# Kernel optimization log

Measured on AMD Instinct MI355X. Metric: run time of the kernel, lower is better.

The kernel has to match this reference:

```python
import jax, jax.numpy as jnp
import numpy as np

G, C_PER, C_IN, J, B, H, W, K = 8, 32, 256, 64, 16, 56, 56, 3


def setup_inputs() -> dict:
    key = jax.random.key(0)
    kx, kw, kb = jax.random.split(key, 3)
    x = jax.random.normal(kx, (B, C_IN, H, W), dtype=jnp.float32)
    # Per-cluster conv weights [G, j_rank, c, K, K] and biases [G, j_rank]
    weight = jax.random.normal(kw, (G, J, C_PER, K, K), dtype=jnp.float32) * 0.05
    bias = jax.random.normal(kb, (G, J), dtype=jnp.float32) * 0.01
    # Arrangements: 8 clusters of 32 non-contiguous channel indices (fixed permutation)
    arrangements = jnp.asarray(
        np.random.RandomState(0).permutation(C_IN).reshape(G, C_PER), dtype=jnp.int32
    )
    return {"x": x, "weight": weight, "bias": bias, "arrangements": arrangements}


def reference(x, weight, bias, arrangements):
    # Gather channel subsets: x[:, arr] -> [B, G, c, H, W] -> [G, B, c, H, W]
    xg = jnp.transpose(x[:, arrangements], (1, 0, 2, 3, 4))

    def conv1(xi, wi):
        # xi: [B, c, H, W], wi: [J, c, K, K]; stride 1, pad 1, dilation 1 (torch default cross-correlation)
        return jax.lax.conv_general_dilated(
            xi, wi,
            window_strides=(1, 1),
            padding=((1, 1), (1, 1)),
            dimension_numbers=("NCHW", "OIHW", "NCHW"),
        )

    out = jax.vmap(conv1)(xg, weight)              # [G, B, J, H, W]
    out = out + bias[:, None, :, None, None]
    g, b, j, h, w = out.shape
    # torch.cat(dim=1) over clusters -> [B, G*J, H, W]
    return jnp.transpose(out, (1, 0, 2, 3, 4)).reshape(b, g * j, h, w)
```

## Files before the change

### kernel.cpp

```cpp
#include <hip/hip_runtime.h>


#define NG 8
#define CPER 32
#define CIN 256
#define NJ 64
#define NB 16
#define NH 56
#define NW 56
#define PXST 40
#define BUFSH (4 * 58 * PXST)
#define NPACK (16 * 4 * 58)
#define NITER 15
#define WEI_SH (9 * 2048)

typedef __attribute__((ext_vector_type(8))) short short8v;
typedef __attribute__((ext_vector_type(4))) float float4v;

__device__ __forceinline__ unsigned bf16rne(float f) {
    unsigned u = __float_as_uint(f);
    return (u + 0x7FFFu + ((u >> 16) & 1u)) >> 16;
}

__global__ __launch_bounds__(256, 2)
void gconv_mfma(const float* __restrict__ x,
                const float* __restrict__ w,
                const float* __restrict__ bias,
                const int* __restrict__ arr,
                float* __restrict__ out) {
    __shared__ __align__(16) unsigned short smem[2 * BUFSH];

    const int tid   = threadIdx.x;
    const int chunk = blockIdx.x;
    const int b     = blockIdx.y;
    const int g     = blockIdx.z;
    const int lane  = tid & 63;
    const int jt    = tid >> 6;
    const int n     = lane & 15;
    const int kq    = lane >> 4;

    {
        const float* wg = w + (size_t)g * (NJ * CPER * 9);
        for (int e = tid; e < WEI_SH; e += 256) {
            int jc = e / 9, tap = e - jc * 9;
            smem[tap * 2048 + jc] = (unsigned short)bf16rne(wg[e]);
        }
    }
    __syncthreads();
    short8v A[9];
    {
        const unsigned short* wl = smem + (jt * 16 + n) * CPER + kq * 8;
        #pragma unroll
        for (int t = 0; t < 9; ++t) A[t] = *(const short8v*)(wl + t * 2048);
    }
    float4v binit;
    #pragma unroll
    for (int i = 0; i < 4; ++i) binit[i] = bias[g * NJ + jt * 16 + kq * 4 + i];
    __syncthreads();

    int pre0[NITER], pre1[NITER], meta[NITER];
    #pragma unroll
    for (int k = 0; k < NITER; ++k) {
        int e = tid + 256 * k;
        int act = e < NPACK;
        int c2 = e / 232;
        int rem = e - c2 * 232;
        int row = rem / 58;
        int colp = rem - row * 58;
        int ch0 = 0, ch1 = 0;
        if (act) { ch0 = arr[g * CPER + c2 * 2]; ch1 = arr[g * CPER + c2 * 2 + 1]; }
        pre0[k] = ch0 * (NH * NW) + (row - 1) * NW + (colp - 1);
        pre1[k] = ch1 * (NH * NW) + (row - 1) * NW + (colp - 1);
        int cv = act && ((unsigned)(colp - 1) < NW);
        meta[k] = ((row * 58 + colp) * PXST + c2 * 2) | (row << 14) | (cv << 16) | (act << 17);
    }
    const float* xb = x + (size_t)b * (CIN * NH * NW);

    float f0[NITER], f1[NITER];
    int r0 = chunk * 14;

    {
        int roff = r0 * NW;
        #pragma unroll
        for (int k = 0; k < NITER; ++k) {
            int row = (meta[k] >> 14) & 3;
            int v = ((meta[k] >> 16) & 1) && ((unsigned)(r0 + row - 1) < NH);
            f0[k] = v ? xb[pre0[k] + roff] : 0.0f;
            f1[k] = v ? xb[pre1[k] + roff] : 0.0f;
        }
        #pragma unroll
        for (int k = 0; k < NITER; ++k) {
            if ((meta[k] >> 17) & 1)
                *(unsigned*)(&smem[meta[k] & 0x3FFF]) =
                    bf16rne(f0[k]) | (bf16rne(f1[k]) << 16);
        }
    }
    __syncthreads();

    for (int bd = 0; bd < 7; ++bd) {
        if (bd < 6) {
            int r1 = r0 + 2, roff = r1 * NW;
            #pragma unroll
            for (int k = 0; k < NITER; ++k) {
                int row = (meta[k] >> 14) & 3;
                int v = ((meta[k] >> 16) & 1) && ((unsigned)(r1 + row - 1) < NH);
                f0[k] = v ? xb[pre0[k] + roff] : 0.0f;
                f1[k] = v ? xb[pre1[k] + roff] : 0.0f;
            }
        }
        {
            const unsigned short* buf = smem + (bd & 1) * BUFSH;
            const int obase = ((b * (NG * NJ) + g * NJ + jt * 16 + kq * 4) * NH + r0) * NW;
            int rl = 0, col = n;
            #pragma unroll
            for (int tp = 0; tp < 3; ++tp) {
                int rlA = rl, colA = col; col += 16; if (col >= NW) { col -= NW; ++rl; }
                int rlB = rl, colB = col; col += 16; if (col >= NW) { col -= NW; ++rl; }
                const unsigned short* pA = buf + (rlA * 58 + colA) * PXST + kq * 8;
                const unsigned short* pB = buf + (rlB * 58 + colB) * PXST + kq * 8;
                float4v a0 = binit, a1 = binit;
                #pragma unroll
                for (int kh = 0; kh < 3; ++kh)
                    #pragma unroll
                    for (int kw = 0; kw < 3; ++kw) {
                        short8v b0 = *(const short8v*)(pA + (kh * 58 + kw) * PXST);
                        short8v b1 = *(const short8v*)(pB + (kh * 58 + kw) * PXST);
                        a0 = __builtin_amdgcn_mfma_f32_16x16x32_bf16(A[kh * 3 + kw], b0, a0, 0, 0, 0);
                        a1 = __builtin_amdgcn_mfma_f32_16x16x32_bf16(A[kh * 3 + kw], b1, a1, 0, 0, 0);
                    }
                int obA = obase + rlA * NW + colA;
                int obB = obase + rlB * NW + colB;
                #pragma unroll
                for (int i = 0; i < 4; ++i) {
                    out[obA + i * (NH * NW)] = a0[i];
                    out[obB + i * (NH * NW)] = a1[i];
                }
            }
            const unsigned short* pA = buf + (rl * 58 + col) * PXST + kq * 8;
            float4v a0 = binit;
            #pragma unroll
            for (int kh = 0; kh < 3; ++kh)
                #pragma unroll
                for (int kw = 0; kw < 3; ++kw) {
                    short8v b0 = *(const short8v*)(pA + (kh * 58 + kw) * PXST);
                    a0 = __builtin_amdgcn_mfma_f32_16x16x32_bf16(A[kh * 3 + kw], b0, a0, 0, 0, 0);
                }
            int obA = obase + rl * NW + col;
            #pragma unroll
            for (int i = 0; i < 4; ++i) out[obA + i * (NH * NW)] = a0[i];
        }
        if (bd < 6) {
            unsigned short* dst = smem + ((bd + 1) & 1) * BUFSH;
            #pragma unroll
            for (int k = 0; k < NITER; ++k) {
                if ((meta[k] >> 17) & 1)
                    *(unsigned*)(&dst[meta[k] & 0x3FFF]) =
                        bf16rne(f0[k]) | (bf16rne(f1[k]) << 16);
            }
            r0 += 2;
            __syncthreads();
        }
    }
}

extern "C" void kernel_launch(void* const* d_in, const int* in_sizes, int n_in,
                              void* d_out, int out_size, void* d_ws, size_t ws_size,
                              hipStream_t stream) {
    const float* x    = (const float*)d_in[0];
    const float* wght = (const float*)d_in[1];
    const float* bias = (const float*)d_in[2];
    const int*   arr  = (const int*)d_in[3];
    float* out = (float*)d_out;

    dim3 grid(4, NB, NG);
    gconv_mfma<<<grid, 256, 0, stream>>>(x, wght, bias, arr, out);
}
```

Before: 183.3 us.

## Use 8-slot row ring buffer with float4 loads and finer row chunks

Replaces the double-buffered 4-row tile with an 8-slot circular row buffer, so each iteration loads only two new input rows instead of reloading the overlapping halo rows. Input loads switch from scalar gathers to float4 vector loads, and column padding is zeroed once up front. The grid grows from 4 to 7 row chunks per image (8 rows each) and launch bounds are raised to 4 blocks per CU to improve occupancy. Outputs are written with nontemporal stores. The risks are higher register pressure under the tighter launch bound and more blocks each repeating the weight load into shared memory.

```diff
diff --git a/kernel.cpp b/kernel.cpp
--- a/kernel.cpp
+++ b/kernel.cpp
@@ -9,9 +9,8 @@
 #define NH 56
 #define NW 56
 #define PXST 40
-#define BUFSH (4 * 58 * PXST)
-#define NPACK (16 * 4 * 58)
-#define NITER 15
+#define SLOT_SH (58 * PXST)
+#define RING_SH (8 * SLOT_SH)
 #define WEI_SH (9 * 2048)
 
 typedef __attribute__((ext_vector_type(8))) short short8v;
@@ -22,13 +21,13 @@
     return (u + 0x7FFFu + ((u >> 16) & 1u)) >> 16;
 }
 
-__global__ __launch_bounds__(256, 2)
+__global__ __launch_bounds__(256, 4)
 void gconv_mfma(const float* __restrict__ x,
                 const float* __restrict__ w,
                 const float* __restrict__ bias,
                 const int* __restrict__ arr,
                 float* __restrict__ out) {
-    __shared__ __align__(16) unsigned short smem[2 * BUFSH];
+    __shared__ __align__(16) unsigned short smem[RING_SH];
 
     const int tid   = threadIdx.x;
     const int chunk = blockIdx.x;
@@ -38,6 +37,7 @@
     const int jt    = tid >> 6;
     const int n     = lane & 15;
     const int kq    = lane >> 4;
+    const int rbase = chunk * 8;
 
     {
         const float* wg = w + (size_t)g * (NJ * CPER * 9);
@@ -58,106 +58,148 @@
     for (int i = 0; i < 4; ++i) binit[i] = bias[g * NJ + jt * 16 + kq * 4 + i];
     __syncthreads();
 
-    int pre0[NITER], pre1[NITER], meta[NITER];
+    const float* xb = x + (size_t)b * (CIN * NH * NW);
+
+    {
+        int s = tid >> 5, rm = tid & 31;
+        int colsel = (rm >> 4) ? 57 : 0;
+        int c = rm & 15;
+        *(unsigned*)(&smem[s * SLOT_SH + colsel * PXST + c * 2]) = 0u;
+    }
+
     #pragma unroll
-    for (int k = 0; k < NITER; ++k) {
-        int e = tid + 256 * k;
-        int act = e < NPACK;
-        int c2 = e / 232;
-        int rem = e - c2 * 232;
-        int row = rem / 58;
-        int colp = rem - row * 58;
-        int ch0 = 0, ch1 = 0;
-        if (act) { ch0 = arr[g * CPER + c2 * 2]; ch1 = arr[g * CPER + c2 * 2 + 1]; }
-        pre0[k] = ch0 * (NH * NW) + (row - 1) * NW + (colp - 1);
-        pre1[k] = ch1 * (NH * NW) + (row - 1) * NW + (colp - 1);
-        int cv = act && ((unsigned)(colp - 1) < NW);
-        meta[k] = ((row * 58 + colp) * PXST + c2 * 2) | (row << 14) | (cv << 16) | (act << 17);
-    }
-    const float* xb = x + (size_t)b * (CIN * NH * NW);
-
-    float f0[NITER], f1[NITER];
-    int r0 = chunk * 14;
-
-    {
-        int roff = r0 * NW;
-        #pragma unroll
-        for (int k = 0; k < NITER; ++k) {
-            int row = (meta[k] >> 14) & 3;
-            int v = ((meta[k] >> 16) & 1) && ((unsigned)(r0 + row - 1) < NH);
-            f0[k] = v ? xb[pre0[k] + roff] : 0.0f;
-            f1[k] = v ? xb[pre1[k] + roff] : 0.0f;
-        }
-        #pragma unroll
-        for (int k = 0; k < NITER; ++k) {
-            if ((meta[k] >> 17) & 1)
-                *(unsigned*)(&smem[meta[k] & 0x3FFF]) =
-                    bf16rne(f0[k]) | (bf16rne(f1[k]) << 16);
-        }
-    }
+    for (int k = 0; k < 4; ++k) {
+        int t = tid + 256 * k;
+        if (t < 896) {
+            int c2 = t / 56, rem = t - c2 * 56;
+            int r4 = rem / 14, gc = rem - r4 * 14;
+            int ch0 = arr[g * CPER + 2 * c2], ch1 = arr[g * CPER + 2 * c2 + 1];
+            int row = rbase - 1 + r4;
+            float4v v0 = 0.f, v1 = 0.f;
+            if ((unsigned)row < NH) {
+                v0 = *(const float4v*)(xb + ch0 * (NH * NW) + row * NW + 4 * gc);
+                v1 = *(const float4v*)(xb + ch1 * (NH * NW) + row * NW + 4 * gc);
+            }
+            unsigned short* d = smem + (row & 7) * SLOT_SH + (1 + 4 * gc) * PXST + 2 * c2;
+            #pragma unroll
+            for (int i = 0; i < 4; ++i)
+                *(unsigned*)(d + i * PXST) = bf16rne(v0[i]) | (bf16rne(v1[i]) << 16);
+        }
+    }
+
+    int gof0[2], gof1[2], ldc[2], rho[2];
+    #pragma unroll
+    for (int k = 0; k < 2; ++k) {
+        int t  = tid + 256 * k;
+        int tt = (t < 448) ? t : 0;
+        int c2 = tt / 28, rem = tt - c2 * 28;
+        int rh = rem / 14, gc = rem - rh * 14;
+        gof0[k] = arr[g * CPER + 2 * c2] * (NH * NW) + 4 * gc;
+        gof1[k] = arr[g * CPER + 2 * c2 + 1] * (NH * NW) + 4 * gc;
+        ldc[k]  = (1 + 4 * gc) * PXST + 2 * c2;
+        rho[k]  = rh;
+    }
+    const bool act1 = (tid < 192);
     __syncthreads();
 
-    for (int bd = 0; bd < 7; ++bd) {
-        if (bd < 6) {
-            int r1 = r0 + 2, roff = r1 * NW;
-            #pragma unroll
-            for (int k = 0; k < NITER; ++k) {
-                int row = (meta[k] >> 14) & 3;
-                int v = ((meta[k] >> 16) & 1) && ((unsigned)(r1 + row - 1) < NH);
-                f0[k] = v ? xb[pre0[k] + roff] : 0.0f;
-                f1[k] = v ? xb[pre1[k] + roff] : 0.0f;
-            }
-        }
+    for (int bd = 0; bd < 4; ++bd) {
+        const int r0 = rbase + 2 * bd;
+        const bool dopf = (bd < 3);
+
+        float4v pfa0 = 0.f, pfa1 = 0.f, pfb0 = 0.f, pfb1 = 0.f;
+        if (dopf) {
+            int rowA = r0 + 3 + rho[0];
+            if (rowA < NH) {
+                pfa0 = *(const float4v*)(xb + gof0[0] + rowA * NW);
+                pfa1 = *(const float4v*)(xb + gof1[0] + rowA * NW);
+            }
+            if (act1) {
+                int rowB = r0 + 3 + rho[1];
+                if (rowB < NH) {
+                    pfb0 = *(const float4v*)(xb + gof0[1] + rowB * NW);
+                    pfb1 = *(const float4v*)(xb + gof1[1] + rowB * NW);
+                }
+            }
+        }
+        __builtin_amdgcn_sched_barrier(0);
+
         {
-            const unsigned short* buf = smem + (bd & 1) * BUFSH;
             const int obase = ((b * (NG * NJ) + g * NJ + jt * 16 + kq * 4) * NH + r0) * NW;
-            int rl = 0, col = n;
+            const int sb0 = ((r0 - 1) & 7) * SLOT_SH;
+            const int sb1 = ((r0    ) & 7) * SLOT_SH;
+            const int sb2 = ((r0 + 1) & 7) * SLOT_SH;
+            const int sb3 = ((r0 + 2) & 7) * SLOT_SH;
+            int rl = 0, col = n, coff = n * PXST + kq * 8;
             #pragma unroll
             for (int tp = 0; tp < 3; ++tp) {
-                int rlA = rl, colA = col; col += 16; if (col >= NW) { col -= NW; ++rl; }
-                int rlB = rl, colB = col; col += 16; if (col >= NW) { col -= NW; ++rl; }
-                const unsigned short* pA = buf + (rlA * 58 + colA) * PXST + kq * 8;
-                const unsigned short* pB = buf + (rlB * 58 + colB) * PXST + kq * 8;
+                const int rlA = rl, colA = col, cfA = coff;
+                col += 16; coff += 16 * PXST; if (col >= NW) { col -= NW; coff -= NW * PXST; ++rl; }
+                const int rlB = rl, colB = col, cfB = coff;
+                col += 16; coff += 16 * PXST; if (col >= NW) { col -= NW; coff -= NW * PXST; ++rl; }
+                const unsigned short* a0p = smem + ((rlA ? sb1 : sb0) + cfA);
+                const unsigned short* a1p = smem + ((rlA ? sb2 : sb1) + cfA);
+                const unsigned short* a2p = smem + ((rlA ? sb3 : sb2) + cfA);
+                const unsigned short* b0p = smem + ((rlB ? sb1 : sb0) + cfB);
+                const unsigned short* b1p = smem + ((rlB ? sb2 : sb1) + cfB);
+                const unsigned short* b2p = smem + ((rlB ? sb3 : sb2) + cfB);
                 float4v a0 = binit, a1 = binit;
                 #pragma unroll
-                for (int kh = 0; kh < 3; ++kh)
-                    #pragma unroll
-                    for (int kw = 0; kw < 3; ++kw) {
-                        short8v b0 = *(const short8v*)(pA + (kh * 58 + kw) * PXST);
-                        short8v b1 = *(const short8v*)(pB + (kh * 58 + kw) * PXST);
-                        a0 = __builtin_amdgcn_mfma_f32_16x16x32_bf16(A[kh * 3 + kw], b0, a0, 0, 0, 0);
-                        a1 = __builtin_amdgcn_mfma_f32_16x16x32_bf16(A[kh * 3 + kw], b1, a1, 0, 0, 0);
-                    }
-                int obA = obase + rlA * NW + colA;
-                int obB = obase + rlB * NW + colB;
+                for (int kw = 0; kw < 3; ++kw) {
+                    short8v x0 = *(const short8v*)(a0p + kw * PXST);
+                    short8v y0 = *(const short8v*)(b0p + kw * PXST);
+                    a0 = __builtin_amdgcn_mfma_f32_16x16x32_bf16(A[kw],     x0, a0, 0, 0, 0);
+                    a1 = __builtin_amdgcn_mfma_f32_16x16x32_bf16(A[kw],     y0, a1, 0, 0, 0);
+                    short8v x1 = *(const short8v*)(a1p + kw * PXST);
+                    short8v y1 = *(const short8v*)(b1p + kw * PXST);
+                    a0 = __builtin_amdgcn_mfma_f32_16x16x32_bf16(A[3 + kw], x1, a0, 0, 0, 0);
+                    a1 = __builtin_amdgcn_mfma_f32_16x16x32_bf16(A[3 + kw], y1, a1, 0, 0, 0);
+                    short8v x2 = *(const short8v*)(a2p + kw * PXST);
+                    short8v y2 = *(const short8v*)(b2p + kw * PXST);
+                    a0 = __builtin_amdgcn_mfma_f32_16x16x32_bf16(A[6 + kw], x2, a0, 0, 0, 0);
+                    a1 = __builtin_amdgcn_mfma_f32_16x16x32_bf16(A[6 + kw], y2, a1, 0, 0, 0);
+                }
+                const int obA = obase + rlA * NW + colA;
+                const int obB = obase + rlB * NW + colB;
                 #pragma unroll
                 for (int i = 0; i < 4; ++i) {
-                    out[obA + i * (NH * NW)] = a0[i];
-                    out[obB + i * (NH * NW)] = a1[i];
+                    __builtin_nontemporal_store(a0[i], &out[obA + i * (NH * NW)]);
+                    __builtin_nontemporal_store(a1[i], &out[obB + i * (NH * NW)]);
                 }
             }
-            const unsigned short* pA = buf + (rl * 58 + col) * PXST + kq * 8;
+            const unsigned short* a0p = smem + ((rl ? sb1 : sb0) + coff);
+            const unsigned short* a1p = smem + ((rl ? sb2 : sb1) + coff);
+            const unsigned short* a2p = smem + ((rl ? sb3 : sb2) + coff);
             float4v a0 = binit;
             #pragma unroll
-            for (int kh = 0; kh < 3; ++kh)
-                #pragma unroll
-                for (int kw = 0; kw < 3; ++kw) {
-                    short8v b0 = *(const short8v*)(pA + (kh * 58 + kw) * PXST);
-                    a0 = __builtin_amdgcn_mfma_f32_16x16x32_bf16(A[kh * 3 + kw], b0, a0, 0, 0, 0);
-                }
-            int obA = obase + rl * NW + col;
-            #pragma unroll
-            for (int i = 0; i < 4; ++i) out[obA + i * (NH * NW)] = a0[i];
-        }
-        if (bd < 6) {
-            unsigned short* dst = smem + ((bd + 1) & 1) * BUFSH;
-            #pragma unroll
-            for (int k = 0; k < NITER; ++k) {
-                if ((meta[k] >> 17) & 1)
-                    *(unsigned*)(&dst[meta[k] & 0x3FFF]) =
-                        bf16rne(f0[k]) | (bf16rne(f1[k]) << 16);
-            }
-            r0 += 2;
+            for (int kw = 0; kw < 3; ++kw) {
+                short8v x0 = *(const short8v*)(a0p + kw * PXST);
+                a0 = __builtin_amdgcn_mfma_f32_16x16x32_bf16(A[kw],     x0, a0, 0, 0, 0);
+                short8v x1 = *(const short8v*)(a1p + kw * PXST);
+                a0 = __builtin_amdgcn_mfma_f32_16x16x32_bf16(A[3 + kw], x1, a0, 0, 0, 0);
+                short8v x2 = *(const short8v*)(a2p + kw * PXST);
+                a0 = __builtin_amdgcn_mfma_f32_16x16x32_bf16(A[6 + kw], x2, a0, 0, 0, 0);
+            }
+            const int obA = obase + rl * NW + col;
+            #pragma unroll
+            for (int i = 0; i < 4; ++i)
+                __builtin_nontemporal_store(a0[i], &out[obA + i * (NH * NW)]);
+        }
+
+        if (dopf) {
+            {
+                int rowA = r0 + 3 + rho[0];
+                unsigned short* d = smem + (rowA & 7) * SLOT_SH + ldc[0];
+                #pragma unroll
+                for (int i = 0; i < 4; ++i)
+                    *(unsigned*)(d + i * PXST) = bf16rne(pfa0[i]) | (bf16rne(pfa1[i]) << 16);
+            }
+            if (act1) {
+                int rowB = r0 + 3 + rho[1];
+                unsigned short* d = smem + (rowB & 7) * SLOT_SH + ldc[1];
+                #pragma unroll
+                for (int i = 0; i < 4; ++i)
+                    *(unsigned*)(d + i * PXST) = bf16rne(pfb0[i]) | (bf16rne(pfb1[i]) << 16);
+            }
             __syncthreads();
         }
     }
@@ -172,6 +214,6 @@
     const int*   arr  = (const int*)d_in[3];
     float* out = (float*)d_out;
 
-    dim3 grid(4, NB, NG);
+    dim3 grid(7, NB, NG);
     gconv_mfma<<<grid, 256, 0, stream>>>(x, wght, bias, arr, out);
 }
```

Measured after the change: 178.1 us. 2.8% less time.

## Load whole 8-row band once per block with float4 loads, drop double-buffered pipeline

Applied to the files above, without the earlier changes.

Each block now handles 8 output rows: it stages all 10 halo input rows into LDS with one pass of vectorized float4 global loads, then syncs once. The rolling double-buffered loop over 2-row bands goes away. Each wave now computes two 16-channel output tiles against every B fragment, which doubles MFMA reuse of each LDS read. The grid grows to 7 chunks with launch bounds targeting 3 blocks per CU, trading the previous overlap of global loads with compute for more parallel blocks and fewer barriers, at the cost of more A registers.

```diff
diff --git a/kernel.cpp b/kernel.cpp
--- a/kernel.cpp
+++ b/kernel.cpp
@@ -8,11 +8,13 @@
 #define NB 16
 #define NH 56
 #define NW 56
-#define PXST 40
-#define BUFSH (4 * 58 * PXST)
-#define NPACK (16 * 4 * 58)
-#define NITER 15
+#define PXSH 40
+#define SLOT_SH (58 * PXSH)
+#define NSLOT 10
+#define BUF_SH (NSLOT * SLOT_SH)
 #define WEI_SH (9 * 2048)
+#define NTASK 2240
+#define KMAX 9
 
 typedef __attribute__((ext_vector_type(8))) short short8v;
 typedef __attribute__((ext_vector_type(4))) float float4v;
@@ -22,22 +24,27 @@
     return (u + 0x7FFFu + ((u >> 16) & 1u)) >> 16;
 }
 
-__global__ __launch_bounds__(256, 2)
+#define MFMA __builtin_amdgcn_mfma_f32_16x16x32_bf16
+
+__global__ __launch_bounds__(256, 3)
 void gconv_mfma(const float* __restrict__ x,
                 const float* __restrict__ w,
                 const float* __restrict__ bias,
                 const int* __restrict__ arr,
                 float* __restrict__ out) {
-    __shared__ __align__(16) unsigned short smem[2 * BUFSH];
+    __shared__ __align__(16) unsigned short smem[BUF_SH];
 
     const int tid   = threadIdx.x;
     const int chunk = blockIdx.x;
     const int b     = blockIdx.y;
     const int g     = blockIdx.z;
     const int lane  = tid & 63;
-    const int jt    = tid >> 6;
+    const int wid   = tid >> 6;
     const int n     = lane & 15;
     const int kq    = lane >> 4;
+    const int jh    = wid & 1;
+    const int ph    = wid >> 1;
+    const int rbase = chunk * 8;
 
     {
         const float* wg = w + (size_t)g * (NJ * CPER * 9);
@@ -47,118 +54,129 @@
         }
     }
     __syncthreads();
-    short8v A[9];
-    {
-        const unsigned short* wl = smem + (jt * 16 + n) * CPER + kq * 8;
+    short8v A[2][9];
+    #pragma unroll
+    for (int jt2 = 0; jt2 < 2; ++jt2) {
+        const unsigned short* wl = smem + ((2 * jh + jt2) * 16 + n) * CPER + kq * 8;
         #pragma unroll
-        for (int t = 0; t < 9; ++t) A[t] = *(const short8v*)(wl + t * 2048);
+        for (int t = 0; t < 9; ++t) A[jt2][t] = *(const short8v*)(wl + t * 2048);
     }
-    float4v binit;
+    float4v binit[2];
     #pragma unroll
-    for (int i = 0; i < 4; ++i) binit[i] = bias[g * NJ + jt * 16 + kq * 4 + i];
+    for (int jt2 = 0; jt2 < 2; ++jt2)
+        #pragma unroll
+        for (int i = 0; i < 4; ++i)
+            binit[jt2][i] = bias[g * NJ + (2 * jh + jt2) * 16 + kq * 4 + i];
     __syncthreads();
 
-    int pre0[NITER], pre1[NITER], meta[NITER];
+    for (int z = tid; z < 320; z += 256) {
+        int s = z >> 5, rm = z & 31;
+        int col = (rm >> 4) ? 57 : 0, cd = rm & 15;
+        *(unsigned*)(&smem[s * SLOT_SH + col * PXSH + cd * 2]) = 0u;
+    }
+
+    const float* xb = x + (size_t)b * (CIN * NH * NW);
+    int xo0[KMAX], xo1[KMAX], wof[KMAX];
+    bool vr[KMAX], act[KMAX];
     #pragma unroll
-    for (int k = 0; k < NITER; ++k) {
-        int e = tid + 256 * k;
-        int act = e < NPACK;
-        int c2 = e / 232;
-        int rem = e - c2 * 232;
-        int row = rem / 58;
-        int colp = rem - row * 58;
-        int ch0 = 0, ch1 = 0;
-        if (act) { ch0 = arr[g * CPER + c2 * 2]; ch1 = arr[g * CPER + c2 * 2 + 1]; }
-        pre0[k] = ch0 * (NH * NW) + (row - 1) * NW + (colp - 1);
-        pre1[k] = ch1 * (NH * NW) + (row - 1) * NW + (colp - 1);
-        int cv = act && ((unsigned)(colp - 1) < NW);
-        meta[k] = ((row * 58 + colp) * PXST + c2 * 2) | (row << 14) | (cv << 16) | (act << 17);
+    for (int k = 0; k < KMAX; ++k) {
+        int tk = tid + 256 * k;
+        act[k] = tk < NTASK;
+        int tt = act[k] ? tk : 0;
+        int c2 = tt / 140, rem = tt - c2 * 140;
+        int lr = rem / 14, gc = rem - lr * 14;
+        int irow = rbase - 1 + lr;
+        vr[k] = (unsigned)irow < NH;
+        int ro = irow * NW + 4 * gc;
+        xo0[k] = arr[g * CPER + 2 * c2] * (NH * NW) + ro;
+        xo1[k] = arr[g * CPER + 2 * c2 + 1] * (NH * NW) + ro;
+        wof[k] = lr * SLOT_SH + (1 + 4 * gc) * PXSH + 2 * c2;
     }
-    const float* xb = x + (size_t)b * (CIN * NH * NW);
 
-    float f0[NITER], f1[NITER];
-    int r0 = chunk * 14;
-
-    {
-        int roff = r0 * NW;
-        #pragma unroll
-        for (int k = 0; k < NITER; ++k) {
-            int row = (meta[k] >> 14) & 3;
-            int v = ((meta[k] >> 16) & 1) && ((unsigned)(r0 + row - 1) < NH);
-            f0[k] = v ? xb[pre0[k] + roff] : 0.0f;
-            f1[k] = v ? xb[pre1[k] + roff] : 0.0f;
+    float4v va[2], vb[2];
+    #pragma unroll
+    for (int k = 0; k < 2; ++k) {
+        float4v t0 = 0.f, t1 = 0.f;
+        if (vr[k]) {
+            t0 = *(const float4v*)(xb + xo0[k]);
+            t1 = *(const float4v*)(xb + xo1[k]);
         }
-        #pragma unroll
-        for (int k = 0; k < NITER; ++k) {
-            if ((meta[k] >> 17) & 1)
-                *(unsigned*)(&smem[meta[k] & 0x3FFF]) =
-                    bf16rne(f0[k]) | (bf16rne(f1[k]) << 16);
+        va[k] = t0; vb[k] = t1;
+    }
+    #pragma unroll
+    for (int k = 0; k < KMAX; ++k) {
+        if (act[k]) {
+            unsigned short* d = smem + wof[k];
+            #pragma unroll
+            for (int i = 0; i < 4; ++i)
+                *(unsigned*)(d + i * PXSH) =
+                    bf16rne(va[k & 1][i]) | (bf16rne(vb[k & 1][i]) << 16);
+        }
+        if (k + 2 < KMAX) {
+            int kk = k + 2;
+            float4v t0 = 0.f, t1 = 0.f;
+            if (vr[kk]) {
+                t0 = *(const float4v*)(xb + xo0[kk]);
+                t1 = *(const float4v*)(xb + xo1[kk]);
+            }
+            va[k & 1] = t0; vb[k & 1] = t1;
         }
     }
     __syncthreads();
 
-    for (int bd = 0; bd < 7; ++bd) {
-        if (bd < 6) {
-            int r1 = r0 + 2, roff = r1 * NW;
-            #pragma unroll
-            for (int k = 0; k < NITER; ++k) {
-                int row = (meta[k] >> 14) & 3;
-                int v = ((meta[k] >> 16) & 1) && ((unsigned)(r1 + row - 1) < NH);
-                f0[k] = v ? xb[pre0[k] + roff] : 0.0f;
-                f1[k] = v ? xb[pre1[k] + roff] : 0.0f;
-            }
-        }
-        {
-            const unsigned short* buf = smem + (bd & 1) * BUFSH;
-            const int obase = ((b * (NG * NJ) + g * NJ + jt * 16 + kq * 4) * NH + r0) * NW;
-            int rl = 0, col = n;
-            #pragma unroll
-            for (int tp = 0; tp < 3; ++tp) {
-                int rlA = rl, colA = col; col += 16; if (col >= NW) { col -= NW; ++rl; }
-                int rlB = rl, colB = col; col += 16; if (col >= NW) { col -= NW; ++rl; }
-                const unsigned short* pA = buf + (rlA * 58 + colA) * PXST + kq * 8;
-                const unsigned short* pB = buf + (rlB * 58 + colB) * PXST + kq * 8;
-                float4v a0 = binit, a1 = binit;
-                #pragma unroll
-                for (int kh = 0; kh < 3; ++kh)
-                    #pragma unroll
-                    for (int kw = 0; kw < 3; ++kw) {
-                        short8v b0 = *(const short8v*)(pA + (kh * 58 + kw) * PXST);
-                        short8v b1 = *(const short8v*)(pB + (kh * 58 + kw) * PXST);
-                        a0 = __builtin_amdgcn_mfma_f32_16x16x32_bf16(A[kh * 3 + kw], b0, a0, 0, 0, 0);
-                        a1 = __builtin_amdgcn_mfma_f32_16x16x32_bf16(A[kh * 3 + kw], b1, a1, 0, 0, 0);
-                    }
-                int obA = obase + rlA * NW + colA;
-                int obB = obase + rlB * NW + colB;
-                #pragma unroll
-                for (int i = 0; i < 4; ++i) {
-                    out[obA + i * (NH * NW)] = a0[i];
-                    out[obB + i * (NH * NW)] = a1[i];
-                }
-            }
-            const unsigned short* pA = buf + (rl * 58 + col) * PXST + kq * 8;
-            float4v a0 = binit;
+    #pragma unroll
+    for (int band2 = 0; band2 < 2; ++band2) {
+        const int band = ph * 2 + band2;
+        const int r0 = rbase + 2 * band;
+        const unsigned short* base = smem + (2 * band) * SLOT_SH + kq * 8;
+        const int ob0 = ((b * (NG * NJ) + g * NJ + jh * 32 + kq * 4) * NH + r0) * NW;
+        const int ob1 = ob0 + 16 * NH * NW;
+        int rl = 0, col = n;
+        #pragma unroll
+        for (int tp = 0; tp < 3; ++tp) {
+            const int rlA = rl, colA = col;
+            col += 16; if (col >= NW) { col -= NW; ++rl; }
+            const int rlB = rl, colB = col;
+            col += 16; if (col >= NW) { col -= NW; ++rl; }
+            const unsigned short* pA = base + rlA * SLOT_SH + colA * PXSH;
+            const unsigned short* pB = base + rlB * SLOT_SH + colB * PXSH;
+            float4v a00 = binit[0], a01 = binit[1];
+            float4v a10 = binit[0], a11 = binit[1];
             #pragma unroll
             for (int kh = 0; kh < 3; ++kh)
                 #pragma unroll
                 for (int kw = 0; kw < 3; ++kw) {
-                    short8v b0 = *(const short8v*)(pA + (kh * 58 + kw) * PXST);
-                    a0 = __builtin_amdgcn_mfma_f32_16x16x32_bf16(A[kh * 3 + kw], b0, a0, 0, 0, 0);
+                    short8v x0 = *(const short8v*)(pA + kh * SLOT_SH + kw * PXSH);
+                    short8v y0 = *(const short8v*)(pB + kh * SLOT_SH + kw * PXSH);
+                    a00 = MFMA(A[0][kh * 3 + kw], x0, a00, 0, 0, 0);
+                    a01 = MFMA(A[1][kh * 3 + kw], x0, a01, 0, 0, 0);
+                    a10 = MFMA(A[0][kh * 3 + kw], y0, a10, 0, 0, 0);
+                    a11 = MFMA(A[1][kh * 3 + kw], y0, a11, 0, 0, 0);
                 }
-            int obA = obase + rl * NW + col;
+            const int oA = rlA * NW + colA, oB = rlB * NW + colB;
             #pragma unroll
-            for (int i = 0; i < 4; ++i) out[obA + i * (NH * NW)] = a0[i];
+            for (int i = 0; i < 4; ++i) {
+                out[ob0 + oA + i * (NH * NW)] = a00[i];
+                out[ob1 + oA + i * (NH * NW)] = a01[i];
+                out[ob0 + oB + i * (NH * NW)] = a10[i];
+                out[ob1 + oB + i * (NH * NW)] = a11[i];
+            }
         }
-        if (bd < 6) {
-            unsigned short* dst = smem + ((bd + 1) & 1) * BUFSH;
+        const unsigned short* pA = base + rl * SLOT_SH + col * PXSH;
+        float4v a00 = binit[0], a01 = binit[1];
+        #pragma unroll
+        for (int kh = 0; kh < 3; ++kh)
             #pragma unroll
-            for (int k = 0; k < NITER; ++k) {
-                if ((meta[k] >> 17) & 1)
-                    *(unsigned*)(&dst[meta[k] & 0x3FFF]) =
-                        bf16rne(f0[k]) | (bf16rne(f1[k]) << 16);
+            for (int kw = 0; kw < 3; ++kw) {
+                short8v x0 = *(const short8v*)(pA + kh * SLOT_SH + kw * PXSH);
+                a00 = MFMA(A[0][kh * 3 + kw], x0, a00, 0, 0, 0);
+                a01 = MFMA(A[1][kh * 3 + kw], x0, a01, 0, 0, 0);
             }
-            r0 += 2;
-            __syncthreads();
+        const int oA = rl * NW + col;
+        #pragma unroll
+        for (int i = 0; i < 4; ++i) {
+            out[ob0 + oA + i * (NH * NW)] = a00[i];
+            out[ob1 + oA + i * (NH * NW)] = a01[i];
         }
     }
 }
@@ -172,6 +190,6 @@
     const int*   arr  = (const int*)d_in[3];
     float* out = (float*)d_out;
 
-    dim3 grid(4, NB, NG);
+    dim3 grid(7, NB, NG);
     gconv_mfma<<<grid, 256, 0, stream>>>(x, wght, bias, arr, out);
 }
```

Result: faster. 172.8 us (-5.7%).

## Split rows into smaller blocks with single-stage vectorized channel-packed LDS staging

Applied to the files above, without the earlier changes.

Each block now computes 4 output rows instead of 14, so the grid grows from 4 to 14 row chunks. The double-buffered software pipeline is removed in favour of one staging pass that loads float4 vectors of 8 gathered channels and writes packed bf16 into a channel-plane LDS layout. The weight staging is split into two passes so it fits in the smaller LDS buffer, and launch bounds are raised to 4 blocks per CU. The aim is more occupancy and parallelism plus cheaper, coalesced global loads. In exchange, halo rows are reloaded more often (6 input rows per 4 output rows) and per-block weight setup is repeated across more blocks.

```diff
diff --git a/kernel.cpp b/kernel.cpp
--- a/kernel.cpp
+++ b/kernel.cpp
@@ -8,27 +8,32 @@
 #define NB 16
 #define NH 56
 #define NW 56
-#define PXST 40
-#define BUFSH (4 * 58 * PXST)
-#define NPACK (16 * 4 * 58)
-#define NITER 15
-#define WEI_SH (9 * 2048)
+#define HW (NH * NW)
+#define PLANE_DW 236
+#define SLOT_DW 944
+#define NSLOT 6
+#define BUF_DW (NSLOT * SLOT_DW)
+#define NTASK 336
 
 typedef __attribute__((ext_vector_type(8))) short short8v;
 typedef __attribute__((ext_vector_type(4))) float float4v;
+typedef __attribute__((ext_vector_type(4))) unsigned int uint4v;
 
 __device__ __forceinline__ unsigned bf16rne(float f) {
     unsigned u = __float_as_uint(f);
     return (u + 0x7FFFu + ((u >> 16) & 1u)) >> 16;
 }
 
-__global__ __launch_bounds__(256, 2)
+#define MFMA __builtin_amdgcn_mfma_f32_16x16x32_bf16
+
+__global__ __launch_bounds__(256, 4)
 void gconv_mfma(const float* __restrict__ x,
                 const float* __restrict__ w,
                 const float* __restrict__ bias,
                 const int* __restrict__ arr,
                 float* __restrict__ out) {
-    __shared__ __align__(16) unsigned short smem[2 * BUFSH];
+    __shared__ __align__(16) unsigned int smw[BUF_DW];
+    unsigned short* sms = (unsigned short*)smw;
 
     const int tid   = threadIdx.x;
     const int chunk = blockIdx.x;
@@ -38,127 +43,93 @@
     const int jt    = tid >> 6;
     const int n     = lane & 15;
     const int kq    = lane >> 4;
+    const int rbase = chunk * 4;
 
+    short8v A[9];
     {
         const float* wg = w + (size_t)g * (NJ * CPER * 9);
-        for (int e = tid; e < WEI_SH; e += 256) {
-            int jc = e / 9, tap = e - jc * 9;
-            smem[tap * 2048 + jc] = (unsigned short)bf16rne(wg[e]);
+        #pragma unroll
+        for (int pass = 0; pass < 2; ++pass) {
+            const int t0 = pass ? 5 : 0;
+            const int nt = pass ? 4 : 5;
+            for (int e = tid; e < nt * 2048; e += 256) {
+                int jc = e / nt, dt = e - jc * nt;
+                sms[dt * 2048 + jc] = (unsigned short)bf16rne(wg[jc * 9 + t0 + dt]);
+            }
+            __syncthreads();
+            const unsigned short* wl = sms + (jt * 16 + n) * CPER + kq * 8;
+            #pragma unroll
+            for (int dt = 0; dt < nt; ++dt)
+                A[t0 + dt] = *(const short8v*)(wl + dt * 2048);
+            __syncthreads();
         }
-    }
-    __syncthreads();
-    short8v A[9];
-    {
-        const unsigned short* wl = smem + (jt * 16 + n) * CPER + kq * 8;
-        #pragma unroll
-        for (int t = 0; t < 9; ++t) A[t] = *(const short8v*)(wl + t * 2048);
     }
     float4v binit;
     #pragma unroll
     for (int i = 0; i < 4; ++i) binit[i] = bias[g * NJ + jt * 16 + kq * 4 + i];
+
+    if (tid < 48) {
+        int lr = tid >> 3, rm = tid & 7;
+        int q = rm >> 1, px = (rm & 1) ? 57 : 0;
+        uint4v z = {0u, 0u, 0u, 0u};
+        *(uint4v*)(smw + lr * SLOT_DW + q * PLANE_DW + px * 4) = z;
+    }
+
+    const float* xb = x + (size_t)b * (CIN * HW);
+    const int* ag = arr + g * CPER;
+    auto stage = [&](int t) {
+        int q = t & 3, s = t >> 2;
+        int p4 = s % 14, lr = s / 14;
+        int irow = rbase - 1 + lr;
+        bool v = (unsigned)irow < NH;
+        const float* src = xb + irow * NW + 4 * p4;
+        float4v vv[8];
+        #pragma unroll
+        for (int j = 0; j < 8; ++j) {
+            float4v t0 = {0.f, 0.f, 0.f, 0.f};
+            if (v) t0 = *(const float4v*)(src + ag[8 * q + j] * HW);
+            vv[j] = t0;
+        }
+        unsigned int* d = smw + lr * SLOT_DW + q * PLANE_DW + (1 + 4 * p4) * 4;
+        #pragma unroll
+        for (int i = 0; i < 4; ++i) {
+            uint4v val;
+            #pragma unroll
+            for (int dd = 0; dd < 4; ++dd)
+                val[dd] = bf16rne(vv[2 * dd][i]) | (bf16rne(vv[2 * dd + 1][i]) << 16);
+            *(uint4v*)(d + 4 * i) = val;
+        }
+    };
+    stage(tid);
+    if (tid < NTASK - 256) stage(tid + 256);
     __syncthreads();
 
-    int pre0[NITER], pre1[NITER], meta[NITER];
+    const int ob = ((b * (NG * NJ) + g * NJ + jt * 16 + kq * 4) * NH + rbase) * NW;
+    int rl = 0, col = n;
     #pragma unroll
-    for (int k = 0; k < NITER; ++k) {
-        int e = tid + 256 * k;
-        int act = e < NPACK;
-        int c2 = e / 232;
-        int rem = e - c2 * 232;
-        int row = rem / 58;
-        int colp = rem - row * 58;
-        int ch0 = 0, ch1 = 0;
-        if (act) { ch0 = arr[g * CPER + c2 * 2]; ch1 = arr[g * CPER + c2 * 2 + 1]; }
-        pre0[k] = ch0 * (NH * NW) + (row - 1) * NW + (colp - 1);
-        pre1[k] = ch1 * (NH * NW) + (row - 1) * NW + (colp - 1);
-        int cv = act && ((unsigned)(colp - 1) < NW);
-        meta[k] = ((row * 58 + colp) * PXST + c2 * 2) | (row << 14) | (cv << 16) | (act << 17);
-    }
-    const float* xb = x + (size_t)b * (CIN * NH * NW);
-
-    float f0[NITER], f1[NITER];
-    int r0 = chunk * 14;
-
-    {
-        int roff = r0 * NW;
+    for (int tp = 0; tp < 7; ++tp) {
+        const int rlA = rl, colA = col;
+        col += 16; if (col >= NW) { col -= NW; ++rl; }
+        const int rlB = rl, colB = col;
+        col += 16; if (col >= NW) { col -= NW; ++rl; }
+        const unsigned int* pA = smw + rlA * SLOT_DW + kq * PLANE_DW + colA * 4;
+        const unsigned int* pB = smw + rlB * SLOT_DW + kq * PLANE_DW + colB * 4;
+        float4v a0 = binit, a1 = binit;
         #pragma unroll
-        for (int k = 0; k < NITER; ++k) {
-            int row = (meta[k] >> 14) & 3;
-            int v = ((meta[k] >> 16) & 1) && ((unsigned)(r0 + row - 1) < NH);
-            f0[k] = v ? xb[pre0[k] + roff] : 0.0f;
-            f1[k] = v ? xb[pre1[k] + roff] : 0.0f;
-        }
+        for (int kh = 0; kh < 3; ++kh)
+            #pragma unroll
+            for (int kw = 0; kw < 3; ++kw) {
+                short8v x0 = *(const short8v*)(pA + kh * SLOT_DW + kw * 4);
+                short8v y0 = *(const short8v*)(pB + kh * SLOT_DW + kw * 4);
+                a0 = MFMA(A[kh * 3 + kw], x0, a0, 0, 0, 0);
+                a1 = MFMA(A[kh * 3 + kw], y0, a1, 0, 0, 0);
+            }
+        const int oA = ob + rlA * NW + colA;
+        const int oB = ob + rlB * NW + colB;
         #pragma unroll
-        for (int k = 0; k < NITER; ++k) {
-            if ((meta[k] >> 17) & 1)
-                *(unsigned*)(&smem[meta[k] & 0x3FFF]) =
-                    bf16rne(f0[k]) | (bf16rne(f1[k]) << 16);
-        }
-    }
-    __syncthreads();
-
-    for (int bd = 0; bd < 7; ++bd) {
-        if (bd < 6) {
-            int r1 = r0 + 2, roff = r1 * NW;
-            #pragma unroll
-            for (int k = 0; k < NITER; ++k) {
-                int row = (meta[k] >> 14) & 3;
-                int v = ((meta[k] >> 16) & 1) && ((unsigned)(r1 + row - 1) < NH);
-                f0[k] = v ? xb[pre0[k] + roff] : 0.0f;
-                f1[k] = v ? xb[pre1[k] + roff] : 0.0f;
-            }
-        }
-        {
-            const unsigned short* buf = smem + (bd & 1) * BUFSH;
-            const int obase = ((b * (NG * NJ) + g * NJ + jt * 16 + kq * 4) * NH + r0) * NW;
-            int rl = 0, col = n;
-            #pragma unroll
-            for (int tp = 0; tp < 3; ++tp) {
-                int rlA = rl, colA = col; col += 16; if (col >= NW) { col -= NW; ++rl; }
-                int rlB = rl, colB = col; col += 16; if (col >= NW) { col -= NW; ++rl; }
-                const unsigned short* pA = buf + (rlA * 58 + colA) * PXST + kq * 8;
-                const unsigned short* pB = buf + (rlB * 58 + colB) * PXST + kq * 8;
-                float4v a0 = binit, a1 = binit;
-                #pragma unroll
-                for (int kh = 0; kh < 3; ++kh)
-                    #pragma unroll
-                    for (int kw = 0; kw < 3; ++kw) {
-                        short8v b0 = *(const short8v*)(pA + (kh * 58 + kw) * PXST);
-                        short8v b1 = *(const short8v*)(pB + (kh * 58 + kw) * PXST);
-                        a0 = __builtin_amdgcn_mfma_f32_16x16x32_bf16(A[kh * 3 + kw], b0, a0, 0, 0, 0);
-                        a1 = __builtin_amdgcn_mfma_f32_16x16x32_bf16(A[kh * 3 + kw], b1, a1, 0, 0, 0);
-                    }
-                int obA = obase + rlA * NW + colA;
-                int obB = obase + rlB * NW + colB;
-                #pragma unroll
-                for (int i = 0; i < 4; ++i) {
-                    out[obA + i * (NH * NW)] = a0[i];
-                    out[obB + i * (NH * NW)] = a1[i];
-                }
-            }
-            const unsigned short* pA = buf + (rl * 58 + col) * PXST + kq * 8;
-            float4v a0 = binit;
-            #pragma unroll
-            for (int kh = 0; kh < 3; ++kh)
-                #pragma unroll
-                for (int kw = 0; kw < 3; ++kw) {
-                    short8v b0 = *(const short8v*)(pA + (kh * 58 + kw) * PXST);
-                    a0 = __builtin_amdgcn_mfma_f32_16x16x32_bf16(A[kh * 3 + kw], b0, a0, 0, 0, 0);
-                }
-            int obA = obase + rl * NW + col;
-            #pragma unroll
-            for (int i = 0; i < 4; ++i) out[obA + i * (NH * NW)] = a0[i];
-        }
-        if (bd < 6) {
-            unsigned short* dst = smem + ((bd + 1) & 1) * BUFSH;
-            #pragma unroll
-            for (int k = 0; k < NITER; ++k) {
-                if ((meta[k] >> 17) & 1)
-                    *(unsigned*)(&dst[meta[k] & 0x3FFF]) =
-                        bf16rne(f0[k]) | (bf16rne(f1[k]) << 16);
-            }
-            r0 += 2;
-            __syncthreads();
+        for (int i = 0; i < 4; ++i) {
+            out[oA + i * HW] = a0[i];
+            out[oB + i * HW] = a1[i];
         }
     }
 }
@@ -172,6 +143,6 @@
     const int*   arr  = (const int*)d_in[3];
     float* out = (float*)d_out;
 
-    dim3 grid(4, NB, NG);
+    dim3 grid(14, NB, NG);
     gconv_mfma<<<grid, 256, 0, stream>>>(x, wght, bias, arr, out);
 }
```

Result: no change. 182.5 us (-0.5%).
